# Kernel tuning notes

Measured on AMD Instinct MI355X. Metric: run time of the kernel, lower is better.

Reference implementation:

```python
import jax, jax.numpy as jnp
import numpy as np

B, N, E, D = 16, 100000, 10, 3


def setup_inputs() -> dict:
    key = jax.random.key(0)
    k1, k2, k3, k4 = jax.random.split(key, 4)
    coord1 = jax.random.normal(k1, (B, N, D), dtype=jnp.float32)
    coord2 = jax.random.normal(k2, (B, N, D), dtype=jnp.float32)
    base = jax.random.randint(k3, (B, N, E), 0, N, dtype=jnp.int64)
    drop = jax.random.uniform(k4, (B, N, E)) < 0.25
    drop = drop.at[:, :, 0].set(False)
    A_list = jnp.where(drop, jnp.int64(-1), base)
    return {"coord1": coord1, "coord2": coord2, "A_list": A_list}


def _centroid(coord, A_list):
    # coord: [B,N,D], A_list: [B,N,E] with -1 for invalid slots
    valid = A_list >= 0                               # [B,N,E]
    idx = jnp.where(valid, A_list, 0)                 # clamp invalid to 0
    # vertices[b,n,e,:] = coord[b, idx[b,n,e], :]
    vertices = jax.vmap(lambda c, i: c[i])(coord, idx)  # [B,N,E,D]
    sum_nb = jnp.sum(vertices * valid[..., None].astype(coord.dtype), axis=2)  # [B,N,D]
    num_nb = jnp.sum(valid.astype(coord.dtype), axis=2, keepdims=True)         # [B,N,1]
    return sum_nb / num_nb


def reference(coord1, coord2, A_list):
    lap1 = coord1 - _centroid(coord1, A_list)
    lap2 = coord2 - _centroid(coord2, A_list)
    # MSELoss(reduction='mean') * num_points
    loss = jnp.mean((lap2 - lap1) ** 2) * coord1.shape[1]
    return loss
```

## Files before the change

### kernel.cpp

```cpp
#include <hip/hip_runtime.h>

constexpr int B = 16;
constexpr int N = 100000;
constexpr int E = 10;
constexpr int D = 3;

__global__ __launch_bounds__(256) void diff_kernel(const float* __restrict__ c1,
                                                   const float* __restrict__ c2,
                                                   float* __restrict__ diff,
                                                   int n4) {
    int i = blockIdx.x * blockDim.x + threadIdx.x;
    if (i < n4) {
        float4 a = reinterpret_cast<const float4*>(c1)[i];
        float4 b = reinterpret_cast<const float4*>(c2)[i];
        float4 d;
        d.x = b.x - a.x; d.y = b.y - a.y; d.z = b.z - a.z; d.w = b.w - a.w;
        reinterpret_cast<float4*>(diff)[i] = d;
    }
}

__global__ __launch_bounds__(256) void loss_kernel(const float* __restrict__ diff,
                                                   const int* __restrict__ A,
                                                   float* __restrict__ out) {
    int per = gridDim.x >> 3;
    int w = (blockIdx.x & 7) * per + (blockIdx.x >> 3);
    int node = w * blockDim.x + threadIdx.x;

    float sq = 0.0f;
    if (node < B * N) {
        int b = node / N;
        int n = node - b * N;
        const float* db = diff + (size_t)b * N * D;

        const int2* a2 = reinterpret_cast<const int2*>(A + (size_t)node * E);
        float sx = 0.f, sy = 0.f, sz = 0.f;
        int cnt = 0;
        #pragma unroll
        for (int e2 = 0; e2 < E / 2; ++e2) {
            int2 p = a2[e2];
            if (p.x >= 0) {
                const float* q = db + (size_t)p.x * D;
                sx += q[0]; sy += q[1]; sz += q[2];
                ++cnt;
            }
            if (p.y >= 0) {
                const float* q = db + (size_t)p.y * D;
                sx += q[0]; sy += q[1]; sz += q[2];
                ++cnt;
            }
        }
        float inv = 1.0f / (float)cnt;
        const float* own = db + (size_t)n * D;
        float lx = own[0] - sx * inv;
        float ly = own[1] - sy * inv;
        float lz = own[2] - sz * inv;
        sq = lx * lx + ly * ly + lz * lz;
    }

    #pragma unroll
    for (int off = 32; off > 0; off >>= 1)
        sq += __shfl_down(sq, off, 64);

    __shared__ float wsum[4];
    int lane = threadIdx.x & 63;
    int wid = threadIdx.x >> 6;
    if (lane == 0) wsum[wid] = sq;
    __syncthreads();
    if (threadIdx.x == 0) {
        float t = (wsum[0] + wsum[1]) + (wsum[2] + wsum[3]);
        atomicAdd(out, t * (1.0f / (float)(B * D)));
    }
}

extern "C" void kernel_launch(void* const* d_in, const int* in_sizes, int n_in,
                              void* d_out, int out_size, void* d_ws, size_t ws_size,
                              hipStream_t stream) {
    const float* coord1 = (const float*)d_in[0];
    const float* coord2 = (const float*)d_in[1];
    const int* A_list = (const int*)d_in[2];
    float* out = (float*)d_out;
    float* diff = (float*)d_ws;

    hipMemsetAsync(out, 0, sizeof(float), stream);

    int total_f = B * N * D;
    int n4 = total_f / 4;
    diff_kernel<<<(n4 + 255) / 256, 256, 0, stream>>>(coord1, coord2, diff, n4);

    int nodes = B * N;
    int nblk = (nodes + 255) / 256;
    nblk = (nblk + 7) & ~7;
    loss_kernel<<<nblk, 256, 0, stream>>>(diff, A_list, out);
}
```

Baseline: 123.1 us.

## Pad diff buffer to float4 per node and batch neighbour gathers branch-free

The difference pass now writes each node's 3-component vector into a 16-byte padded float4 slot, so every neighbour gather in the loss kernel is a single aligned 16-byte load instead of three scalar loads. The loss kernel reads each adjacency row with wide int4/int2 loads and issues all ten gathers unconditionally, with invalid slots clamped to index 0 and masked by a multiply. This is meant to cut gather instruction count and raise memory-level parallelism. In exchange the diff buffer grows by a third, some masked loads are wasted, and the padded path is used only when the workspace is large enough, otherwise a packed fallback runs.

Result: faster. 112.2 us (-8.9%).

```diff
diff --git a/kernel.cpp b/kernel.cpp
--- a/kernel.cpp
+++ b/kernel.cpp
@@ -4,6 +4,27 @@
 constexpr int N = 100000;
 constexpr int E = 10;
 constexpr int D = 3;
+
+__global__ __launch_bounds__(256) void diff4_kernel(const float* __restrict__ c1,
+                                                    const float* __restrict__ c2,
+                                                    float4* __restrict__ diffp,
+                                                    int nquad) {
+    int i = blockIdx.x * blockDim.x + threadIdx.x;
+    if (i >= nquad) return;
+    const float4* a4 = reinterpret_cast<const float4*>(c1) + (size_t)i * 3;
+    const float4* b4 = reinterpret_cast<const float4*>(c2) + (size_t)i * 3;
+    float4 a0 = a4[0], a1 = a4[1], a2 = a4[2];
+    float4 b0 = b4[0], b1 = b4[1], b2 = b4[2];
+    float d[12];
+    d[0] = b0.x - a0.x; d[1] = b0.y - a0.y; d[2] = b0.z - a0.z; d[3] = b0.w - a0.w;
+    d[4] = b1.x - a1.x; d[5] = b1.y - a1.y; d[6] = b1.z - a1.z; d[7] = b1.w - a1.w;
+    d[8] = b2.x - a2.x; d[9] = b2.y - a2.y; d[10] = b2.z - a2.z; d[11] = b2.w - a2.w;
+    float4* o = diffp + (size_t)i * 4;
+    o[0] = make_float4(d[0], d[1], d[2], 0.f);
+    o[1] = make_float4(d[3], d[4], d[5], 0.f);
+    o[2] = make_float4(d[6], d[7], d[8], 0.f);
+    o[3] = make_float4(d[9], d[10], d[11], 0.f);
+}
 
 __global__ __launch_bounds__(256) void diff_kernel(const float* __restrict__ c1,
                                                    const float* __restrict__ c2,
@@ -13,12 +34,12 @@
     if (i < n4) {
         float4 a = reinterpret_cast<const float4*>(c1)[i];
         float4 b = reinterpret_cast<const float4*>(c2)[i];
-        float4 d;
-        d.x = b.x - a.x; d.y = b.y - a.y; d.z = b.z - a.z; d.w = b.w - a.w;
-        reinterpret_cast<float4*>(diff)[i] = d;
+        reinterpret_cast<float4*>(diff)[i] =
+            make_float4(b.x - a.x, b.y - a.y, b.z - a.z, b.w - a.w);
     }
 }
 
+template <bool PAD4>
 __global__ __launch_bounds__(256) void loss_kernel(const float* __restrict__ diff,
                                                    const int* __restrict__ A,
                                                    float* __restrict__ out) {
@@ -29,31 +50,64 @@
     float sq = 0.0f;
     if (node < B * N) {
         int b = node / N;
-        int n = node - b * N;
-        const float* db = diff + (size_t)b * N * D;
+        const int* arow = A + (size_t)node * E;
+        int4 p0 = *reinterpret_cast<const int4*>(arow);
+        int4 p1 = *reinterpret_cast<const int4*>(arow + 4);
+        int2 p2 = *reinterpret_cast<const int2*>(arow + 8);
+        int idx[E] = {p0.x, p0.y, p0.z, p0.w, p1.x, p1.y, p1.z, p1.w, p2.x, p2.y};
 
-        const int2* a2 = reinterpret_cast<const int2*>(A + (size_t)node * E);
         float sx = 0.f, sy = 0.f, sz = 0.f;
-        int cnt = 0;
-        #pragma unroll
-        for (int e2 = 0; e2 < E / 2; ++e2) {
-            int2 p = a2[e2];
-            if (p.x >= 0) {
-                const float* q = db + (size_t)p.x * D;
-                sx += q[0]; sy += q[1]; sz += q[2];
-                ++cnt;
+        float fcnt = 0.f;
+        float lx, ly, lz;
+
+        if (PAD4) {
+            const float4* db = reinterpret_cast<const float4*>(diff) + (size_t)b * N;
+            float4 v[E];
+            float m[E];
+            #pragma unroll
+            for (int e = 0; e < E; ++e) {
+                int ix = idx[e];
+                m[e] = (ix >= 0) ? 1.0f : 0.0f;
+                v[e] = db[ix >= 0 ? ix : 0];
             }
-            if (p.y >= 0) {
-                const float* q = db + (size_t)p.y * D;
-                sx += q[0]; sy += q[1]; sz += q[2];
-                ++cnt;
+            float4 own = db[node - b * N];
+            #pragma unroll
+            for (int e = 0; e < E; ++e) {
+                sx = fmaf(v[e].x, m[e], sx);
+                sy = fmaf(v[e].y, m[e], sy);
+                sz = fmaf(v[e].z, m[e], sz);
+                fcnt += m[e];
             }
+            float inv = 1.0f / fcnt;
+            lx = own.x - sx * inv;
+            ly = own.y - sy * inv;
+            lz = own.z - sz * inv;
+        } else {
+            const float* db = diff + (size_t)b * N * D;
+            float vx[E], vy[E], vz[E], m[E];
+            #pragma unroll
+            for (int e = 0; e < E; ++e) {
+                int ix = idx[e];
+                m[e] = (ix >= 0) ? 1.0f : 0.0f;
+                const float* q = db + (size_t)(ix >= 0 ? ix : 0) * D;
+                float2 xy = *reinterpret_cast<const float2*>(q);
+                vx[e] = xy.x; vy[e] = xy.y; vz[e] = q[2];
+            }
+            int n = node - b * N;
+            const float* ownp = db + (size_t)n * D;
+            float ox = ownp[0], oy = ownp[1], oz = ownp[2];
+            #pragma unroll
+            for (int e = 0; e < E; ++e) {
+                sx = fmaf(vx[e], m[e], sx);
+                sy = fmaf(vy[e], m[e], sy);
+                sz = fmaf(vz[e], m[e], sz);
+                fcnt += m[e];
+            }
+            float inv = 1.0f / fcnt;
+            lx = ox - sx * inv;
+            ly = oy - sy * inv;
+            lz = oz - sz * inv;
         }
-        float inv = 1.0f / (float)cnt;
-        const float* own = db + (size_t)n * D;
-        float lx = own[0] - sx * inv;
-        float ly = own[1] - sy * inv;
-        float lz = own[2] - sz * inv;
         sq = lx * lx + ly * ly + lz * lz;
     }
 
@@ -83,12 +137,23 @@
 
     hipMemsetAsync(out, 0, sizeof(float), stream);
 
-    int total_f = B * N * D;
-    int n4 = total_f / 4;
-    diff_kernel<<<(n4 + 255) / 256, 256, 0, stream>>>(coord1, coord2, diff, n4);
+    const size_t pad4_bytes = (size_t)B * N * 4 * sizeof(float);
+    const bool pad4 = ws_size >= pad4_bytes;
 
     int nodes = B * N;
+    if (pad4) {
+        int nquad = nodes / 4;
+        diff4_kernel<<<(nquad + 255) / 256, 256, 0, stream>>>(
+            coord1, coord2, (float4*)diff, nquad);
+    } else {
+        int n4 = nodes * D / 4;
+        diff_kernel<<<(n4 + 255) / 256, 256, 0, stream>>>(coord1, coord2, diff, n4);
+    }
+
     int nblk = (nodes + 255) / 256;
     nblk = (nblk + 7) & ~7;
-    loss_kernel<<<nblk, 256, 0, stream>>>(diff, A_list, out);
+    if (pad4)
+        loss_kernel<true><<<nblk, 256, 0, stream>>>(diff, A_list, out);
+    else
+        loss_kernel<false><<<nblk, 256, 0, stream>>>(diff, A_list, out);
 }
```
